# Kernel tuning notes

Hardware: AMD Instinct MI355X
Metric: run time of the kernel (lower is better)

The kernel has to match this reference:

```python
import jax, jax.numpy as jnp
import numpy as np

D_MODEL = 1024
D_STATE = 128
SEQ_LEN = 4096
BATCH = 4
N_FFT = 2 ** int(np.ceil(np.log2(2 * SEQ_LEN - 1)))  # 8192
LN_EPS = 1e-3  # keras LayerNormalization default epsilon


def setup_inputs() -> dict:
    key = jax.random.key(0)
    ks = jax.random.split(key, 12)
    def dense_w(k, fan_in, fan_out):
        lim = np.sqrt(6.0 / (fan_in + fan_out)).astype(np.float32)  # glorot uniform
        return jax.random.uniform(k, (fan_in, fan_out), jnp.float32, -lim, lim)
    return {
        "x": jax.random.normal(ks[0], (BATCH, SEQ_LEN, D_MODEL), jnp.float32),
        "ln_gamma": jnp.ones((D_MODEL,), jnp.float32),
        "ln_beta": jnp.zeros((D_MODEL,), jnp.float32),
        "W_in": dense_w(ks[1], D_MODEL, D_MODEL),
        "b_in": jnp.zeros((D_MODEL,), jnp.float32),
        "W_xs": dense_w(ks[2], D_MODEL, D_STATE),
        "W_B": dense_w(ks[3], D_MODEL, D_STATE),
        "b_B": jnp.zeros((D_STATE,), jnp.float32),
        "W_C": dense_w(ks[4], D_MODEL, D_STATE),
        "b_C": jnp.zeros((D_STATE,), jnp.float32),
        "A_log": jax.random.uniform(ks[5], (D_STATE,), jnp.float32, -4.0, -1.0),
        "D": jnp.ones((D_MODEL,), jnp.float32),
        "W_so": dense_w(ks[6], D_STATE, D_MODEL),
        "W_out": dense_w(ks[7], D_MODEL, D_MODEL),
        "b_out": jnp.zeros((D_MODEL,), jnp.float32),
    }


def reference(x, ln_gamma, ln_beta, W_in, b_in, W_xs, W_B, b_B, W_C, b_C,
              A_log, D, W_so, W_out, b_out):
    residual = x
    # LayerNorm over last dim
    mu = jnp.mean(x, axis=-1, keepdims=True)
    var = jnp.mean(jnp.square(x - mu), axis=-1, keepdims=True)
    xn = (x - mu) * jax.lax.rsqrt(var + LN_EPS) * ln_gamma + ln_beta
    # projections
    z = xn @ W_in + b_in                      # [B, L, d_model]
    x_state = z @ W_xs                        # [B, L, d_state]
    B_sel = z @ W_B + b_B                     # [B, L, d_state]
    C_sel = z @ W_C + b_C                     # [B, L, d_state]
    # stable A-parameterization -> kernel K[t, s] = exp(A_s * t)
    A = -jnp.exp(A_log)                       # [d_state]
    t = jnp.arange(SEQ_LEN, dtype=jnp.float32)
    K = jnp.exp(t[:, None] * A[None, :])      # [L, d_state]
    # FFT convolution along time axis (zero-padded to N_FFT, causal slice)
    u = x_state * B_sel                       # [B, L, d_state]
    u_f = jnp.fft.rfft(u, n=N_FFT, axis=1)    # [B, N_FFT//2+1, d_state]
    k_f = jnp.fft.rfft(K, n=N_FFT, axis=0)    # [N_FFT//2+1, d_state]
    y_state = jnp.fft.irfft(u_f * k_f[None], n=N_FFT, axis=1)[:, :SEQ_LEN]
    y_state = y_state * C_sel
    # output path with skip connection through D
    y = y_state @ W_so + D * z                # [B, L, d_model]
    y = y @ W_out + b_out
    return y + residual
```

## Files before the change

### kernel.cpp

```cpp
#include <hip/hip_runtime.h>
#include <math.h>

#define D_MODEL 1024
#define D_STATE 128
#define SEQ_LEN 4096
#define BATCH 4
#define NTOK (BATCH * SEQ_LEN)
#define LN_EPS 1e-3f
#define NCHUNK 128
#define LCHUNK (SEQ_LEN / NCHUNK)

typedef __attribute__((ext_vector_type(8))) short bf16x8;
typedef __attribute__((ext_vector_type(4))) float f32x4;

__device__ __forceinline__ short f2bf(float f) {
    union { float f; unsigned u; } v; v.f = f;
    unsigned r = v.u + 0x7FFFu + ((v.u >> 16) & 1u);
    return (short)(r >> 16);
}
__device__ __forceinline__ float bf2f(short s) {
    union { unsigned u; float f; } v; v.u = ((unsigned)(unsigned short)s) << 16;
    return v.f;
}

__global__ __launch_bounds__(256) void ln_kernel(const float* __restrict__ x,
                                                 const float* __restrict__ gamma,
                                                 const float* __restrict__ beta,
                                                 short* __restrict__ xn_bf) {
    int row = blockIdx.x;
    const float4* xr = (const float4*)(x + (size_t)row * D_MODEL);
    float4 v = xr[threadIdx.x];
    float s1 = v.x + v.y + v.z + v.w;
    float s2 = v.x * v.x + v.y * v.y + v.z * v.z + v.w * v.w;
    for (int off = 32; off; off >>= 1) {
        s1 += __shfl_down(s1, off);
        s2 += __shfl_down(s2, off);
    }
    __shared__ float ls1[4], ls2[4];
    int wid = threadIdx.x >> 6, lane = threadIdx.x & 63;
    if (lane == 0) { ls1[wid] = s1; ls2[wid] = s2; }
    __syncthreads();
    s1 = ls1[0] + ls1[1] + ls1[2] + ls1[3];
    s2 = ls2[0] + ls2[1] + ls2[2] + ls2[3];
    float mu = s1 * (1.0f / D_MODEL);
    float var = s2 * (1.0f / D_MODEL) - mu * mu;
    float r = rsqrtf(var + LN_EPS);
    float4 g = ((const float4*)gamma)[threadIdx.x];
    float4 b = ((const float4*)beta)[threadIdx.x];
    short4 o;
    o.x = f2bf((v.x - mu) * r * g.x + b.x);
    o.y = f2bf((v.y - mu) * r * g.y + b.y);
    o.z = f2bf((v.z - mu) * r * g.z + b.z);
    o.w = f2bf((v.w - mu) * r * g.w + b.w);
    ((short4*)(xn_bf + (size_t)row * D_MODEL))[threadIdx.x] = o;
}

__global__ __launch_bounds__(256) void prep_kernel(
    const float* __restrict__ W_in, const float* __restrict__ W_xs,
    const float* __restrict__ W_B, const float* __restrict__ W_C,
    const float* __restrict__ W_so, const float* __restrict__ W_out,
    const float* __restrict__ bB, const float* __restrict__ bC,
    short* __restrict__ W_inT, short* __restrict__ W3T,
    short* __restrict__ W_soT, short* __restrict__ W_outT,
    float* __restrict__ bias3) {
    int blk = blockIdx.x;
    const float* in; short* out; int K, N, tile;
    if (blk < 1024)      { in = W_in;  out = W_inT;           K = 1024; N = 1024; tile = blk; }
    else if (blk < 1152) { in = W_xs;  out = W3T;             K = 1024; N = 128;  tile = blk - 1024; }
    else if (blk < 1280) { in = W_B;   out = W3T + 128*1024;  K = 1024; N = 128;  tile = blk - 1152; }
    else if (blk < 1408) { in = W_C;   out = W3T + 256*1024;  K = 1024; N = 128;  tile = blk - 1280; }
    else if (blk < 1536) { in = W_so;  out = W_soT;           K = 128;  N = 1024; tile = blk - 1408; }
    else if (blk < 2560) { in = W_out; out = W_outT;          K = 1024; N = 1024; tile = blk - 1536; }
    else {
        int t = threadIdx.y * 32 + threadIdx.x;
        for (int n = t; n < 384; n += 256)
            bias3[n] = (n < 128) ? 0.f : ((n < 256) ? bB[n - 128] : bC[n - 256]);
        return;
    }
    __shared__ float t32[32][33];
    int ntiles = N / 32;
    int nb = (tile % ntiles) * 32, kb = (tile / ntiles) * 32;
    int tx = threadIdx.x, ty = threadIdx.y;
#pragma unroll
    for (int i = 0; i < 4; ++i)
        t32[ty + 8 * i][tx] = in[(size_t)(kb + ty + 8 * i) * N + nb + tx];
    __syncthreads();
#pragma unroll
    for (int i = 0; i < 4; ++i)
        out[(size_t)(nb + ty + 8 * i) * K + kb + tx] = f2bf(t32[tx][ty + 8 * i]);
}

template<int HAS_BIAS, int HAS_ADD, int ADD_BF, int HAS_SCALE, int OUT_F32, int OUT_BF, int SWZ>
__global__ __launch_bounds__(256, 4) void gemm_bf16(
    const short* __restrict__ A, const short* __restrict__ BT,
    const float* __restrict__ bias,
    const float* __restrict__ addf, const short* __restrict__ addb,
    const float* __restrict__ addscale,
    float* __restrict__ Cf, short* __restrict__ Cbf,
    int Mt, int Nt, int K) {
    __shared__ short As[128 * 64];
    __shared__ short Bs[128 * 64];
    int p = blockIdx.x;
    int mtile, ntile;
    if (SWZ) {
        int k = p & 7, q = p >> 3;
        ntile = q & 7;
        mtile = k + 8 * (q >> 3);
    } else {
        mtile = p % Mt;
        ntile = p / Mt;
    }
    int m0 = mtile * 128, n0 = ntile * 128;
    int N = Nt * 128;
    int tid = threadIdx.x;
    int lane = tid & 63;
    int w = tid >> 6;
    int quad = lane >> 4, r16 = lane & 15;
    int wm = (w & 1) * 64, wn = (w >> 1) * 64;

    f32x4 acc[4][4] = {};

    for (int k0 = 0; k0 < K; k0 += 64) {
#pragma unroll
        for (int it = 0; it < 4; ++it) {
            int seg = it * 256 + tid;
            int row = seg >> 3, slot = seg & 7;
            int kc8 = slot ^ (row & 7);
            const short* gp = A + (size_t)(m0 + row) * K + k0 + kc8 * 8;
            __builtin_amdgcn_global_load_lds(
                (const __attribute__((address_space(1))) unsigned*)gp,
                (__attribute__((address_space(3))) unsigned*)(As + seg * 8), 16, 0, 0);
        }
#pragma unroll
        for (int it = 0; it < 4; ++it) {
            int seg = it * 256 + tid;
            int row = seg >> 3, slot = seg & 7;
            int kc8 = slot ^ (row & 7);
            const short* gp = BT + (size_t)(n0 + row) * K + k0 + kc8 * 8;
            __builtin_amdgcn_global_load_lds(
                (const __attribute__((address_space(1))) unsigned*)gp,
                (__attribute__((address_space(3))) unsigned*)(Bs + seg * 8), 16, 0, 0);
        }
        __syncthreads();

        const short* abase = As + (wm + r16) * 64;
        const short* bbase = Bs + (wn + r16) * 64;
        int sw = r16 & 7;
#pragma unroll
        for (int kk = 0; kk < 2; ++kk) {
            int phys = ((quad + 4 * kk) ^ sw) * 8;
            bf16x8 af[4], bfr[4];
#pragma unroll
            for (int i = 0; i < 4; ++i) af[i] = *(const bf16x8*)(abase + i * 16 * 64 + phys);
#pragma unroll
            for (int j = 0; j < 4; ++j) bfr[j] = *(const bf16x8*)(bbase + j * 16 * 64 + phys);
#pragma unroll
            for (int i = 0; i < 4; ++i)
#pragma unroll
                for (int j = 0; j < 4; ++j)
                    acc[i][j] = __builtin_amdgcn_mfma_f32_16x16x32_bf16(af[i], bfr[j], acc[i][j], 0, 0, 0);
        }
        __syncthreads();
    }

#pragma unroll
    for (int i = 0; i < 4; ++i) {
#pragma unroll
        for (int j = 0; j < 4; ++j) {
            int col = n0 + wn + j * 16 + r16;
            float bv = HAS_BIAS ? bias[col] : 0.f;
            float sc = HAS_SCALE ? addscale[col] : 1.f;
#pragma unroll
            for (int pr = 0; pr < 4; ++pr) {
                int row = m0 + wm + i * 16 + quad * 4 + pr;
                float v = acc[i][j][pr] + bv;
                if (HAS_ADD) {
                    float av = ADD_BF ? bf2f(addb[(size_t)row * N + col])
                                      : addf[(size_t)row * N + col];
                    v += sc * av;
                }
                if (OUT_F32) Cf[(size_t)row * N + col] = v;
                if (OUT_BF) Cbf[(size_t)row * N + col] = f2bf(v);
            }
        }
    }
}

__global__ __launch_bounds__(128) void scan_p1(const float* __restrict__ s3,
                                               const float* __restrict__ A_log,
                                               float* __restrict__ hbuf,
                                               float* __restrict__ Ebuf) {
    int s = threadIdx.x;
    int c = blockIdx.x, b = blockIdx.y;
    float a = expf(-expf(A_log[s]));
    float h = 0.f;
    size_t base = (size_t)b * SEQ_LEN + (size_t)c * LCHUNK;
#pragma unroll 8
    for (int i = 0; i < LCHUNK; ++i) {
        size_t r = base + i;
        float u = s3[r * 384 + s] * s3[r * 384 + 128 + s];
        h = a * h + u;
        hbuf[r * 128 + s] = h;
    }
    Ebuf[((size_t)b * NCHUNK + c) * 128 + s] = h;
}

__global__ __launch_bounds__(512) void scan_p2(const float* __restrict__ A_log,
                                               const float* __restrict__ Ebuf,
                                               float* __restrict__ Gbuf) {
    int tid = threadIdx.x;
    int b = tid >> 7, s = tid & 127;
    float pw = expf(-expf(A_log[s]) * (float)LCHUNK);
    float G = 0.f;
    for (int c0 = 0; c0 < NCHUNK; c0 += 16) {
        float e[16];
#pragma unroll
        for (int t = 0; t < 16; ++t)
            e[t] = Ebuf[((size_t)b * NCHUNK + c0 + t) * 128 + s];
#pragma unroll
        for (int t = 0; t < 16; ++t) {
            G = pw * G + e[t];
            Gbuf[((size_t)b * NCHUNK + c0 + t) * 128 + s] = G;
        }
    }
}

__global__ __launch_bounds__(128) void scan_p3(const float* __restrict__ s3,
                                               const float* __restrict__ A_log,
                                               const float* __restrict__ hbuf,
                                               const float* __restrict__ Gbuf,
                                               short* __restrict__ ys_bf) {
    int s = threadIdx.x;
    int c = blockIdx.x, b = blockIdx.y;
    float a = expf(-expf(A_log[s]));
    float carry = (c == 0) ? 0.f : Gbuf[((size_t)b * NCHUNK + c - 1) * 128 + s];
    float p = a;
    size_t base = (size_t)b * SEQ_LEN + (size_t)c * LCHUNK;
#pragma unroll 8
    for (int i = 0; i < LCHUNK; ++i) {
        size_t r = base + i;
        float h = hbuf[r * 128 + s] + p * carry;
        p *= a;
        ys_bf[r * 128 + s] = f2bf(h * s3[r * 384 + 256 + s]);
    }
}

extern "C" void kernel_launch(void* const* d_in, const int* in_sizes, int n_in,
                              void* d_out, int out_size, void* d_ws, size_t ws_size,
                              hipStream_t stream) {
    const float* x     = (const float*)d_in[0];
    const float* ln_g  = (const float*)d_in[1];
    const float* ln_b  = (const float*)d_in[2];
    const float* W_in  = (const float*)d_in[3];
    const float* b_in  = (const float*)d_in[4];
    const float* W_xs  = (const float*)d_in[5];
    const float* W_B   = (const float*)d_in[6];
    const float* b_B   = (const float*)d_in[7];
    const float* W_C   = (const float*)d_in[8];
    const float* b_C   = (const float*)d_in[9];
    const float* A_log = (const float*)d_in[10];
    const float* Dvec  = (const float*)d_in[11];
    const float* W_so  = (const float*)d_in[12];
    const float* W_out = (const float*)d_in[13];
    const float* b_out = (const float*)d_in[14];
    float* out = (float*)d_out;

    char* w = (char*)d_ws;
    size_t off = 0;
    short* xn_bf = (short*)(w + off);
    float* hbuf  = (float*)(w + off);
    short* ys_bf = (short*)(w + off + 8388608);
    off += (size_t)NTOK * D_MODEL * 2;
    short* z_bf  = (short*)(w + off);
    off += (size_t)NTOK * D_MODEL * 2;
    short* y1_bf = (short*)(w + off);
    off += (size_t)NTOK * D_MODEL * 2;
    float* s3    = (float*)(w + off); off += (size_t)NTOK * 384 * 4;
    float* Ebuf  = (float*)(w + off); off += (size_t)BATCH * NCHUNK * 128 * 4;
    float* Gbuf  = (float*)(w + off); off += (size_t)BATCH * NCHUNK * 128 * 4;
    short* W_inT  = (short*)(w + off); off += (size_t)D_MODEL * D_MODEL * 2;
    short* W3T    = (short*)(w + off); off += (size_t)384 * D_MODEL * 2;
    short* W_soT  = (short*)(w + off); off += (size_t)D_MODEL * D_STATE * 2;
    short* W_outT = (short*)(w + off); off += (size_t)D_MODEL * D_MODEL * 2;
    float* bias3  = (float*)(w + off); off += 2048;

    prep_kernel<<<2561, dim3(32, 8), 0, stream>>>(W_in, W_xs, W_B, W_C, W_so, W_out,
                                                  b_B, b_C, W_inT, W3T, W_soT, W_outT, bias3);

    ln_kernel<<<NTOK, 256, 0, stream>>>(x, ln_g, ln_b, xn_bf);

    const int Mt = NTOK / 128;
    gemm_bf16<1, 0, 0, 0, 0, 1, 1><<<Mt * 8, 256, 0, stream>>>(
        xn_bf, W_inT, b_in, nullptr, nullptr, nullptr,
        nullptr, z_bf, Mt, 8, D_MODEL);

    gemm_bf16<1, 0, 0, 0, 1, 0, 0><<<Mt * 3, 256, 0, stream>>>(
        z_bf, W3T, bias3, nullptr, nullptr, nullptr,
        s3, nullptr, Mt, 3, D_MODEL);

    scan_p1<<<dim3(NCHUNK, BATCH), 128, 0, stream>>>(s3, A_log, hbuf, Ebuf);
    scan_p2<<<1, 512, 0, stream>>>(A_log, Ebuf, Gbuf);
    scan_p3<<<dim3(NCHUNK, BATCH), 128, 0, stream>>>(s3, A_log, hbuf, Gbuf, ys_bf);

    gemm_bf16<0, 1, 1, 1, 0, 1, 1><<<Mt * 8, 256, 0, stream>>>(
        ys_bf, W_soT, nullptr, nullptr, z_bf, Dvec,
        nullptr, y1_bf, Mt, 8, D_STATE);

    gemm_bf16<1, 1, 0, 0, 1, 0, 1><<<Mt * 8, 256, 0, stream>>>(
        y1_bf, W_outT, b_out, x, nullptr, nullptr,
        out, nullptr, Mt, 8, D_MODEL);
}
```

Measured before the change: 284.2 us.

## Fuse three-pass chunked scan into single-pass decoupled-lookback kernel; merge LN and prep

Replaces the three scan kernels (chunk local scan, serial carry scan, fixup) with one kernel. It uses a ticket-ordered decoupled lookback, so chunk-local states stay in registers instead of round-tripping through the hbuf workspace. The LayerNorm and weight-transpose/prep kernels are merged into a single launch. This removes launches and the hbuf write/read traffic, but adds a memset, spin-waiting on flags, and higher register pressure from a 32-element per-thread array.

```diff
diff --git a/kernel.cpp b/kernel.cpp
--- a/kernel.cpp
+++ b/kernel.cpp
@@ -23,39 +23,9 @@
     return v.f;
 }
 
-__global__ __launch_bounds__(256) void ln_kernel(const float* __restrict__ x,
-                                                 const float* __restrict__ gamma,
-                                                 const float* __restrict__ beta,
-                                                 short* __restrict__ xn_bf) {
-    int row = blockIdx.x;
-    const float4* xr = (const float4*)(x + (size_t)row * D_MODEL);
-    float4 v = xr[threadIdx.x];
-    float s1 = v.x + v.y + v.z + v.w;
-    float s2 = v.x * v.x + v.y * v.y + v.z * v.z + v.w * v.w;
-    for (int off = 32; off; off >>= 1) {
-        s1 += __shfl_down(s1, off);
-        s2 += __shfl_down(s2, off);
-    }
-    __shared__ float ls1[4], ls2[4];
-    int wid = threadIdx.x >> 6, lane = threadIdx.x & 63;
-    if (lane == 0) { ls1[wid] = s1; ls2[wid] = s2; }
-    __syncthreads();
-    s1 = ls1[0] + ls1[1] + ls1[2] + ls1[3];
-    s2 = ls2[0] + ls2[1] + ls2[2] + ls2[3];
-    float mu = s1 * (1.0f / D_MODEL);
-    float var = s2 * (1.0f / D_MODEL) - mu * mu;
-    float r = rsqrtf(var + LN_EPS);
-    float4 g = ((const float4*)gamma)[threadIdx.x];
-    float4 b = ((const float4*)beta)[threadIdx.x];
-    short4 o;
-    o.x = f2bf((v.x - mu) * r * g.x + b.x);
-    o.y = f2bf((v.y - mu) * r * g.y + b.y);
-    o.z = f2bf((v.z - mu) * r * g.z + b.z);
-    o.w = f2bf((v.w - mu) * r * g.w + b.w);
-    ((short4*)(xn_bf + (size_t)row * D_MODEL))[threadIdx.x] = o;
-}
-
-__global__ __launch_bounds__(256) void prep_kernel(
+__global__ __launch_bounds__(256) void pre_kernel(
+    const float* __restrict__ x, const float* __restrict__ gamma,
+    const float* __restrict__ beta, short* __restrict__ xn_bf,
     const float* __restrict__ W_in, const float* __restrict__ W_xs,
     const float* __restrict__ W_B, const float* __restrict__ W_C,
     const float* __restrict__ W_so, const float* __restrict__ W_out,
@@ -63,7 +33,36 @@
     short* __restrict__ W_inT, short* __restrict__ W3T,
     short* __restrict__ W_soT, short* __restrict__ W_outT,
     float* __restrict__ bias3) {
-    int blk = blockIdx.x;
+    if (blockIdx.x < NTOK) {
+        int row = blockIdx.x;
+        const float4* xr = (const float4*)(x + (size_t)row * D_MODEL);
+        float4 v = xr[threadIdx.x];
+        float s1 = v.x + v.y + v.z + v.w;
+        float s2 = v.x * v.x + v.y * v.y + v.z * v.z + v.w * v.w;
+        for (int off = 32; off; off >>= 1) {
+            s1 += __shfl_down(s1, off);
+            s2 += __shfl_down(s2, off);
+        }
+        __shared__ float ls1[4], ls2[4];
+        int wid = threadIdx.x >> 6, lane = threadIdx.x & 63;
+        if (lane == 0) { ls1[wid] = s1; ls2[wid] = s2; }
+        __syncthreads();
+        s1 = ls1[0] + ls1[1] + ls1[2] + ls1[3];
+        s2 = ls2[0] + ls2[1] + ls2[2] + ls2[3];
+        float mu = s1 * (1.0f / D_MODEL);
+        float var = s2 * (1.0f / D_MODEL) - mu * mu;
+        float r = rsqrtf(var + LN_EPS);
+        float4 g = ((const float4*)gamma)[threadIdx.x];
+        float4 b = ((const float4*)beta)[threadIdx.x];
+        short4 o;
+        o.x = f2bf((v.x - mu) * r * g.x + b.x);
+        o.y = f2bf((v.y - mu) * r * g.y + b.y);
+        o.z = f2bf((v.z - mu) * r * g.z + b.z);
+        o.w = f2bf((v.w - mu) * r * g.w + b.w);
+        ((short4*)(xn_bf + (size_t)row * D_MODEL))[threadIdx.x] = o;
+        return;
+    }
+    int blk = blockIdx.x - NTOK;
     const float* in; short* out; int K, N, tile;
     if (blk < 1024)      { in = W_in;  out = W_inT;           K = 1024; N = 1024; tile = blk; }
     else if (blk < 1152) { in = W_xs;  out = W3T;             K = 1024; N = 128;  tile = blk - 1024; }
@@ -72,7 +71,7 @@
     else if (blk < 1536) { in = W_so;  out = W_soT;           K = 128;  N = 1024; tile = blk - 1408; }
     else if (blk < 2560) { in = W_out; out = W_outT;          K = 1024; N = 1024; tile = blk - 1536; }
     else {
-        int t = threadIdx.y * 32 + threadIdx.x;
+        int t = threadIdx.x;
         for (int n = t; n < 384; n += 256)
             bias3[n] = (n < 128) ? 0.f : ((n < 256) ? bB[n - 128] : bC[n - 256]);
         return;
@@ -80,7 +79,7 @@
     __shared__ float t32[32][33];
     int ntiles = N / 32;
     int nb = (tile % ntiles) * 32, kb = (tile / ntiles) * 32;
-    int tx = threadIdx.x, ty = threadIdx.y;
+    int tx = threadIdx.x & 31, ty = threadIdx.x >> 5;
 #pragma unroll
     for (int i = 0; i < 4; ++i)
         t32[ty + 8 * i][tx] = in[(size_t)(kb + ty + 8 * i) * N + nb + tx];
@@ -186,62 +185,90 @@
     }
 }
 
-__global__ __launch_bounds__(128) void scan_p1(const float* __restrict__ s3,
-                                               const float* __restrict__ A_log,
-                                               float* __restrict__ hbuf,
-                                               float* __restrict__ Ebuf) {
+#define FLAG_AGG 1
+#define FLAG_INC 2
+__global__ __launch_bounds__(128) void scan_fused(
+    const float* __restrict__ s3, const float* __restrict__ A_log,
+    float* __restrict__ Ebuf, float* __restrict__ Gbuf,
+    int* __restrict__ flags, int* __restrict__ ticket,
+    short* __restrict__ ys_bf) {
+    __shared__ int sh;
     int s = threadIdx.x;
-    int c = blockIdx.x, b = blockIdx.y;
-    float a = expf(-expf(A_log[s]));
-    float h = 0.f;
+    if (s == 0)
+        sh = __hip_atomic_fetch_add(ticket, 1, __ATOMIC_RELAXED, __HIP_MEMORY_SCOPE_AGENT);
+    __syncthreads();
+    int rank = sh;
+    __syncthreads();
+    int b = rank >> 7;
+    int c = rank & (NCHUNK - 1);
+
+    float A = -expf(A_log[s]);
+    float a = expf(A);
+    float pw = expf(A * (float)LCHUNK);
     size_t base = (size_t)b * SEQ_LEN + (size_t)c * LCHUNK;
-#pragma unroll 8
+
+    float h[LCHUNK];
+    float hh = 0.f;
+#pragma unroll
     for (int i = 0; i < LCHUNK; ++i) {
         size_t r = base + i;
         float u = s3[r * 384 + s] * s3[r * 384 + 128 + s];
-        h = a * h + u;
-        hbuf[r * 128 + s] = h;
-    }
-    Ebuf[((size_t)b * NCHUNK + c) * 128 + s] = h;
-}
-
-__global__ __launch_bounds__(512) void scan_p2(const float* __restrict__ A_log,
-                                               const float* __restrict__ Ebuf,
-                                               float* __restrict__ Gbuf) {
-    int tid = threadIdx.x;
-    int b = tid >> 7, s = tid & 127;
-    float pw = expf(-expf(A_log[s]) * (float)LCHUNK);
-    float G = 0.f;
-    for (int c0 = 0; c0 < NCHUNK; c0 += 16) {
-        float e[16];
-#pragma unroll
-        for (int t = 0; t < 16; ++t)
-            e[t] = Ebuf[((size_t)b * NCHUNK + c0 + t) * 128 + s];
-#pragma unroll
-        for (int t = 0; t < 16; ++t) {
-            G = pw * G + e[t];
-            Gbuf[((size_t)b * NCHUNK + c0 + t) * 128 + s] = G;
-        }
-    }
-}
-
-__global__ __launch_bounds__(128) void scan_p3(const float* __restrict__ s3,
-                                               const float* __restrict__ A_log,
-                                               const float* __restrict__ hbuf,
-                                               const float* __restrict__ Gbuf,
-                                               short* __restrict__ ys_bf) {
-    int s = threadIdx.x;
-    int c = blockIdx.x, b = blockIdx.y;
-    float a = expf(-expf(A_log[s]));
-    float carry = (c == 0) ? 0.f : Gbuf[((size_t)b * NCHUNK + c - 1) * 128 + s];
-    float p = a;
-    size_t base = (size_t)b * SEQ_LEN + (size_t)c * LCHUNK;
-#pragma unroll 8
+        hh = a * hh + u;
+        h[i] = hh;
+    }
+    float E = hh;
+    size_t idx = ((size_t)b * NCHUNK + c) * 128 + s;
+    float carry = 0.f;
+
+    if (c == 0) {
+        __hip_atomic_store(&Gbuf[idx], E, __ATOMIC_RELAXED, __HIP_MEMORY_SCOPE_AGENT);
+        __syncthreads();
+        if (s == 0)
+            __hip_atomic_store(&flags[b * NCHUNK], FLAG_INC, __ATOMIC_RELEASE, __HIP_MEMORY_SCOPE_AGENT);
+    } else {
+        __hip_atomic_store(&Ebuf[idx], E, __ATOMIC_RELAXED, __HIP_MEMORY_SCOPE_AGENT);
+        __syncthreads();
+        if (s == 0)
+            __hip_atomic_store(&flags[b * NCHUNK + c], FLAG_AGG, __ATOMIC_RELEASE, __HIP_MEMORY_SCOPE_AGENT);
+        float pwk = 1.f;
+        int j = c - 1;
+        while (true) {
+            if (s == 0) {
+                int f;
+                do {
+                    f = __hip_atomic_load(&flags[b * NCHUNK + j], __ATOMIC_ACQUIRE, __HIP_MEMORY_SCOPE_AGENT);
+                } while (f == 0);
+                sh = f;
+            }
+            __syncthreads();
+            int f = sh;
+            __syncthreads();
+            size_t jdx = ((size_t)b * NCHUNK + j) * 128 + s;
+            if (f == FLAG_INC) {
+                float G = __hip_atomic_load(&Gbuf[jdx], __ATOMIC_RELAXED, __HIP_MEMORY_SCOPE_AGENT);
+                carry += pwk * G;
+                break;
+            } else {
+                float Ej = __hip_atomic_load(&Ebuf[jdx], __ATOMIC_RELAXED, __HIP_MEMORY_SCOPE_AGENT);
+                carry += pwk * Ej;
+                pwk *= pw;
+                --j;
+            }
+        }
+        float G = E + pw * carry;
+        __hip_atomic_store(&Gbuf[idx], G, __ATOMIC_RELAXED, __HIP_MEMORY_SCOPE_AGENT);
+        __syncthreads();
+        if (s == 0)
+            __hip_atomic_store(&flags[b * NCHUNK + c], FLAG_INC, __ATOMIC_RELEASE, __HIP_MEMORY_SCOPE_AGENT);
+    }
+
+    float ap = a;
+#pragma unroll
     for (int i = 0; i < LCHUNK; ++i) {
         size_t r = base + i;
-        float h = hbuf[r * 128 + s] + p * carry;
-        p *= a;
-        ys_bf[r * 128 + s] = f2bf(h * s3[r * 384 + 256 + s]);
+        float hv = h[i] + ap * carry;
+        ap *= a;
+        ys_bf[r * 128 + s] = f2bf(hv * s3[r * 384 + 256 + s]);
     }
 }
 
@@ -268,7 +295,6 @@
     char* w = (char*)d_ws;
     size_t off = 0;
     short* xn_bf = (short*)(w + off);
-    float* hbuf  = (float*)(w + off);
     short* ys_bf = (short*)(w + off + 8388608);
     off += (size_t)NTOK * D_MODEL * 2;
     short* z_bf  = (short*)(w + off);
@@ -278,16 +304,20 @@
     float* s3    = (float*)(w + off); off += (size_t)NTOK * 384 * 4;
     float* Ebuf  = (float*)(w + off); off += (size_t)BATCH * NCHUNK * 128 * 4;
     float* Gbuf  = (float*)(w + off); off += (size_t)BATCH * NCHUNK * 128 * 4;
+    int*   scanctl = (int*)(w + off); off += 4096;
     short* W_inT  = (short*)(w + off); off += (size_t)D_MODEL * D_MODEL * 2;
     short* W3T    = (short*)(w + off); off += (size_t)384 * D_MODEL * 2;
     short* W_soT  = (short*)(w + off); off += (size_t)D_MODEL * D_STATE * 2;
     short* W_outT = (short*)(w + off); off += (size_t)D_MODEL * D_MODEL * 2;
     float* bias3  = (float*)(w + off); off += 2048;
-
-    prep_kernel<<<2561, dim3(32, 8), 0, stream>>>(W_in, W_xs, W_B, W_C, W_so, W_out,
-                                                  b_B, b_C, W_inT, W3T, W_soT, W_outT, bias3);
-
-    ln_kernel<<<NTOK, 256, 0, stream>>>(x, ln_g, ln_b, xn_bf);
+    int* flags  = scanctl;
+    int* ticket = scanctl + BATCH * NCHUNK;
+
+    hipMemsetAsync(scanctl, 0, 4096, stream);
+
+    pre_kernel<<<NTOK + 2561, 256, 0, stream>>>(
+        x, ln_g, ln_b, xn_bf, W_in, W_xs, W_B, W_C, W_so, W_out,
+        b_B, b_C, W_inT, W3T, W_soT, W_outT, bias3);
 
     const int Mt = NTOK / 128;
     gemm_bf16<1, 0, 0, 0, 0, 1, 1><<<Mt * 8, 256, 0, stream>>>(
@@ -298,9 +328,8 @@
         z_bf, W3T, bias3, nullptr, nullptr, nullptr,
         s3, nullptr, Mt, 3, D_MODEL);
 
-    scan_p1<<<dim3(NCHUNK, BATCH), 128, 0, stream>>>(s3, A_log, hbuf, Ebuf);
-    scan_p2<<<1, 512, 0, stream>>>(A_log, Ebuf, Gbuf);
-    scan_p3<<<dim3(NCHUNK, BATCH), 128, 0, stream>>>(s3, A_log, hbuf, Gbuf, ys_bf);
+    scan_fused<<<BATCH * NCHUNK, 128, 0, stream>>>(s3, A_log, Ebuf, Gbuf,
+                                                   flags, ticket, ys_bf);
 
     gemm_bf16<0, 1, 1, 1, 0, 1, 1><<<Mt * 8, 256, 0, stream>>>(
         ys_bf, W_soT, nullptr, nullptr, z_bf, Dvec,
```

Result: slower. 386.3 us (+36.0%).
